# Kernel tuning notes

Measured on AMD Instinct MI355X. Metric: run time of the kernel, lower is better.

Reference implementation:

```python
import jax, jax.numpy as jnp
import numpy as np

# ---- Cl(4,1) Cayley table (conformal GA: metric +,+,+,+,-) ----
_METRIC = (1.0, 1.0, 1.0, 1.0, -1.0)

def _reorder_sign(a, b):
    # sign from counting swaps to bring blade product to canonical order
    a >>= 1
    s = 0
    while a:
        s += bin(a & b).count("1")
        a >>= 1
    return -1.0 if (s & 1) else 1.0

def _build_cayley():
    C = np.zeros((32, 32, 32), dtype=np.float32)
    for a in range(32):
        for b in range(32):
            s = _reorder_sign(a, b)
            common = a & b
            for i in range(5):
                if (common >> i) & 1:
                    s *= _METRIC[i]
            C[a, b, a ^ b] += s
    return C

CAYLEY = _build_cayley()  # [32,32,32]; out_k = sum_ij C[i,j,k] x_i y_j

EPS = 1e-8

def normalize_cl41(x):
    n = jnp.sqrt(jnp.sum(x * x, axis=-1, keepdims=True))
    return x / (n + EPS)


def setup_inputs() -> dict:
    key = jax.random.key(0)
    k_x, k_wi, k_bi, k_wo, k_bo = jax.random.split(key, 5)
    B, S, D, H = 64, 2048, 6, 8
    x = jax.random.normal(k_x, (B, S, D), dtype=jnp.float32)
    W_in = jax.random.normal(k_wi, (D, H * 32), dtype=jnp.float32) * (1.0 / np.sqrt(D))
    b_in = jax.random.normal(k_bi, (H * 32,), dtype=jnp.float32) * 0.01
    W_out = jax.random.normal(k_wo, (H * 32, 32), dtype=jnp.float32) * (1.0 / np.sqrt(H * 32))
    b_out = jax.random.normal(k_bo, (32,), dtype=jnp.float32) * 0.01
    return {"x": x, "W_in": W_in, "b_in": b_in, "W_out": W_out, "b_out": b_out}


def reference(x, W_in, b_in, W_out, b_out):
    B, S, D = x.shape
    H = W_in.shape[1] // 32
    C = jnp.asarray(CAYLEY)
    # project inputs to per-channel multivectors: (B,S,H,32)
    u = (x @ W_in + b_in).reshape(B, S, H, 32)
    # initial rotor state: identity (scalar blade = 1)
    psi0 = jnp.zeros((B, H, 32), dtype=x.dtype).at[..., 0].set(1.0)

    def step(psi, u_t):  # u_t: (B,H,32)
        delta = normalize_cl41(u_t.at[..., 0].add(1.0))
        psi = normalize_cl41(jnp.einsum("bhi,bhj,ijk->bhk", delta, psi, C))
        return psi, psi

    _, psi_seq = jax.lax.scan(step, psi0, jnp.swapaxes(u, 0, 1))  # (S,B,H,32)
    out = normalize_cl41(psi_seq.reshape(S, B, H * 32) @ W_out + b_out)  # (S,B,32)
    return jnp.swapaxes(out, 0, 1)  # (B,S,32)
```

## Files before the change

kernel.cpp:

```cpp
#include <hip/hip_runtime.h>
#include <hip/hip_bf16.h>
#include <stdint.h>

#define BB 64
#define SS 2048
#define DD 6
#define HH 8
#define NCH 512
#define CHUNKS 256
#define LCH 8

typedef unsigned short ushort_t;
typedef __attribute__((ext_vector_type(8))) __bf16 bf16x8;
typedef __attribute__((ext_vector_type(4))) float f32x4;

struct SignTab { float s[32][32]; };

constexpr int popc5_c(unsigned v) {
    int c = 0;
    for (int i = 0; i < 5; ++i) c += (v >> i) & 1u;
    return c;
}

constexpr SignTab make_signs() {
    SignTab t{};
    for (int a = 0; a < 32; ++a) {
        for (int b = 0; b < 32; ++b) {
            int cnt = 0;
            unsigned aa = ((unsigned)a) >> 1;
            while (aa) { cnt += popc5_c(aa & (unsigned)b); aa >>= 1; }
            if ((a & b) & 16) cnt += 1;
            t.s[a][b] = (cnt & 1) ? -1.0f : 1.0f;
        }
    }
    return t;
}

constexpr SignTab SGN = make_signs();

__device__ __forceinline__ void gp_cl41(const float* __restrict__ a,
                                        const float* __restrict__ b,
                                        float* __restrict__ o) {
#pragma unroll
    for (int k = 0; k < 32; ++k) o[k] = 0.0f;
#pragma unroll
    for (int i = 0; i < 32; ++i) {
#pragma unroll
        for (int k = 0; k < 32; ++k) {
            o[k] = fmaf(SGN.s[i][i ^ k] * a[i], b[i ^ k], o[k]);
        }
    }
}

__device__ __forceinline__ float sumsq32(const float* v) {
    float n0 = 0.f, n1 = 0.f, n2 = 0.f, n3 = 0.f;
#pragma unroll
    for (int k = 0; k < 32; k += 4) {
        n0 = fmaf(v[k+0], v[k+0], n0);
        n1 = fmaf(v[k+1], v[k+1], n1);
        n2 = fmaf(v[k+2], v[k+2], n2);
        n3 = fmaf(v[k+3], v[k+3], n3);
    }
    return (n0 + n1) + (n2 + n3);
}

__device__ __forceinline__ float rsq(float n) {
    return __builtin_amdgcn_rsqf(n);
}

__device__ __forceinline__ uint32_t f2bf_rne(float f) {
    uint32_t u = __float_as_uint(f);
    return (u + 0x7FFFu + ((u >> 16) & 1u)) >> 16;
}

__device__ __forceinline__ void make_delta2(const float4* __restrict__ sW,
                                            const float* __restrict__ xv,
                                            float* __restrict__ dl0,
                                            float* __restrict__ dl1) {
#pragma unroll
    for (int j4 = 0; j4 < 8; ++j4) {
        float4 bv = sW[48 + j4];
        dl0[4*j4+0] = bv.x; dl0[4*j4+1] = bv.y; dl0[4*j4+2] = bv.z; dl0[4*j4+3] = bv.w;
        dl1[4*j4+0] = bv.x; dl1[4*j4+1] = bv.y; dl1[4*j4+2] = bv.z; dl1[4*j4+3] = bv.w;
    }
#pragma unroll
    for (int d = 0; d < 6; ++d) {
        float a0 = xv[d], a1 = xv[6 + d];
#pragma unroll
        for (int j4 = 0; j4 < 8; ++j4) {
            float4 w = sW[d * 8 + j4];
            dl0[4*j4+0] = fmaf(a0, w.x, dl0[4*j4+0]);
            dl0[4*j4+1] = fmaf(a0, w.y, dl0[4*j4+1]);
            dl0[4*j4+2] = fmaf(a0, w.z, dl0[4*j4+2]);
            dl0[4*j4+3] = fmaf(a0, w.w, dl0[4*j4+3]);
            dl1[4*j4+0] = fmaf(a1, w.x, dl1[4*j4+0]);
            dl1[4*j4+1] = fmaf(a1, w.y, dl1[4*j4+1]);
            dl1[4*j4+2] = fmaf(a1, w.z, dl1[4*j4+2]);
            dl1[4*j4+3] = fmaf(a1, w.w, dl1[4*j4+3]);
        }
    }
    dl0[0] += 1.0f;
    dl1[0] += 1.0f;
}

__device__ __forceinline__ void loadx12(const float* __restrict__ xr, float* __restrict__ xv) {
    const float4* xp = (const float4*)xr;
#pragma unroll
    for (int m = 0; m < 3; ++m) {
        float4 t4 = xp[m];
        xv[4*m] = t4.x; xv[4*m+1] = t4.y; xv[4*m+2] = t4.z; xv[4*m+3] = t4.w;
    }
}

__global__ __launch_bounds__(256, 1) void k_scan(
        const float* __restrict__ x, const float* __restrict__ W_in,
        const float* __restrict__ b_in, float* __restrict__ Ebuf) {
    __shared__ float4 sW4[57];
    __shared__ float sT[CHUNKS][36];

    int chain = blockIdx.x;
    int b = chain >> 3, h = chain & 7;
    int c = threadIdx.x;

    if (c < 56) {
        float4 v;
        if (c < 48) {
            int d = c / 8, j4 = c % 8;
            const float* p = W_in + d * 256 + h * 32 + 4 * j4;
            v = make_float4(p[0], p[1], p[2], p[3]);
        } else {
            const float* p = b_in + h * 32 + 4 * (c - 48);
            v = make_float4(p[0], p[1], p[2], p[3]);
        }
        sW4[c] = v;
    }
    __syncthreads();

    const float* xrow = x + ((size_t)b * SS + (size_t)c * LCH) * DD;
    float P[32], O[32];
    {
        float xv[12];
        loadx12(xrow, xv);
        float dl0[32], dl1[32];
        make_delta2(sW4, xv, dl0, dl1);
        gp_cl41(dl1, dl0, P);
    }
#pragma unroll 1
    for (int pr = 1; pr < 4; ++pr) {
        float xv[12];
        loadx12(xrow + 12 * pr, xv);
        float dl0[32], dl1[32];
        make_delta2(sW4, xv, dl0, dl1);
        gp_cl41(dl0, P, O);
        gp_cl41(dl1, O, P);
    }

    float v[32];
    {
        float inv = rsq(sumsq32(P));
#pragma unroll
        for (int k = 0; k < 32; ++k) v[k] = P[k] * inv;
#pragma unroll
        for (int m = 0; m < 8; ++m)
            *(float4*)&sT[c][4*m] = make_float4(v[4*m], v[4*m+1], v[4*m+2], v[4*m+3]);
    }
    __syncthreads();

#pragma unroll 1
    for (int off = 1; off < CHUNKS; off <<= 1) {
        float w[32];
        bool act = (c >= off);
        if (act) {
#pragma unroll
            for (int m = 0; m < 8; ++m) {
                float4 t4 = *(const float4*)&sT[c - off][4*m];
                w[4*m] = t4.x; w[4*m+1] = t4.y; w[4*m+2] = t4.z; w[4*m+3] = t4.w;
            }
        }
        __syncthreads();
        if (act) {
            gp_cl41(v, w, O);
            float inv = rsq(sumsq32(O));
#pragma unroll
            for (int k = 0; k < 32; ++k) v[k] = O[k] * inv;
#pragma unroll
            for (int m = 0; m < 8; ++m)
                *(float4*)&sT[c][4*m] = make_float4(v[4*m], v[4*m+1], v[4*m+2], v[4*m+3]);
        }
        __syncthreads();
    }

    float* dst = Ebuf + (size_t)chain * CHUNKS * 32;
    if (c == 0) {
        *(float4*)dst = make_float4(1.f, 0.f, 0.f, 0.f);
#pragma unroll
        for (int m = 1; m < 8; ++m) *(float4*)(dst + 4*m) = make_float4(0.f, 0.f, 0.f, 0.f);
    }
    if (c < CHUNKS - 1) {
        float* d2 = dst + (size_t)(c + 1) * 32;
#pragma unroll
        for (int m = 0; m < 8; ++m)
            *(float4*)(d2 + 4*m) = make_float4(v[4*m], v[4*m+1], v[4*m+2], v[4*m+3]);
    }
}

__global__ __launch_bounds__(256, 1) void k_chain_proj(
        const float* __restrict__ x, const float* __restrict__ W_in,
        const float* __restrict__ b_in, const float* __restrict__ Ebuf,
        const float* __restrict__ W_out, const float* __restrict__ b_out,
        float* __restrict__ out) {
    __shared__ float4 sW4[8][57];
    __shared__ float sX[1536];
    __shared__ ushort_t Wt[32 * 256];
    __shared__ ushort_t psiT[4 * 16 * 256];

    int tid = threadIdx.x;
    int wv = tid >> 6, lane = tid & 63;
    int b = blockIdx.x >> 3, gq = blockIdx.x & 7;
    int grp = gq * 4 + wv;
    int c0 = grp * 8;
    int cl = lane >> 3, h = lane & 7;
    int q = lane >> 4, n0 = lane & 15;

    float4 pv[8];
    {
        const float4* ep = (const float4*)(Ebuf +
                (((size_t)b * HH + h) * CHUNKS + (c0 + cl)) * 32);
#pragma unroll
        for (int m = 0; m < 8; ++m) pv[m] = ep[m];
    }

    for (int idx = tid; idx < 448; idx += 256) {
        int hh = idx / 56, r = idx % 56;
        float4 v;
        if (r < 48) {
            int d = r / 8, j4 = r % 8;
            const float* p = W_in + d * 256 + hh * 32 + 4 * j4;
            v = make_float4(p[0], p[1], p[2], p[3]);
        } else {
            const float* p = b_in + hh * 32 + 4 * (r - 48);
            v = make_float4(p[0], p[1], p[2], p[3]);
        }
        sW4[hh][r] = v;
    }

    {
        const float4* xp = (const float4*)(x + ((size_t)b * SS + (size_t)gq * 256) * DD);
        float4* sx4 = (float4*)sX;
        for (int idx = tid; idx < 384; idx += 256) sx4[idx] = xp[idx];
    }

    for (int idx = tid; idx < 2048; idx += 256) {
        int k = idx >> 3, n4 = (idx & 7) << 2;
        float4 w4 = ((const float4*)W_out)[idx];
        ushort_t vals[4] = { (ushort_t)f2bf_rne(w4.x), (ushort_t)f2bf_rne(w4.y),
                             (ushort_t)f2bf_rne(w4.z), (ushort_t)f2bf_rne(w4.w) };
#pragma unroll
        for (int j = 0; j < 4; ++j) {
            int n = n4 + j;
            uint32_t off = (uint32_t)(n * 512 + 2 * k) ^ (uint32_t)((n & 7) << 4);
            *(ushort_t*)((char*)Wt + off) = vals[j];
        }
    }
    __syncthreads();

    float p[32];
#pragma unroll
    for (int m = 0; m < 8; ++m) {
        p[4*m] = pv[m].x; p[4*m+1] = pv[m].y; p[4*m+2] = pv[m].z; p[4*m+3] = pv[m].w;
    }

    bf16x8 Bf[2][8];
#pragma unroll
    for (int nt = 0; nt < 2; ++nt) {
        int n = nt * 16 + n0;
        uint32_t rb = (uint32_t)(n * 512);
        uint32_t sw = (uint32_t)((n & 7) << 4);
#pragma unroll
        for (int kk = 0; kk < 8; ++kk)
            Bf[nt][kk] = *(const bf16x8*)((const char*)Wt + ((rb + kk * 64 + q * 16) ^ sw));
    }
    float bn0 = b_out[n0], bn1 = b_out[16 + n0];

    ushort_t* myT = psiT + wv * 16 * 256;

#pragma unroll 1
    for (int pr = 0; pr < 4; ++pr) {
        float xv[12];
        {
            const float* xr = sX + (wv * 64 + cl * 8 + 2 * pr) * 6;
#pragma unroll
            for (int d = 0; d < 12; ++d) xv[d] = xr[d];
        }

        float dl0[32], dl1[32], o[32];
        make_delta2(sW4[h], xv, dl0, dl1);

        gp_cl41(dl0, p, o);
        {
            float inv = rsq(sumsq32(o));
            int row = cl * 2;
            uint32_t rb = (uint32_t)(row * 512 + h * 64);
            uint32_t sw = (uint32_t)((row & 7) << 4);
            uint32_t pk[16];
#pragma unroll
            for (int m = 0; m < 16; ++m)
                pk[m] = f2bf_rne(o[2*m] * inv) | (f2bf_rne(o[2*m+1] * inv) << 16);
#pragma unroll
            for (int m = 0; m < 4; ++m)
                *(uint4*)((char*)myT + ((rb + 16 * m) ^ sw)) =
                    make_uint4(pk[4*m], pk[4*m+1], pk[4*m+2], pk[4*m+3]);
        }
        gp_cl41(dl1, o, p);
        {
            float inv = rsq(sumsq32(p));
            int row = cl * 2 + 1;
            uint32_t rb = (uint32_t)(row * 512 + h * 64);
            uint32_t sw = (uint32_t)((row & 7) << 4);
            uint32_t pk[16];
#pragma unroll
            for (int m = 0; m < 16; ++m)
                pk[m] = f2bf_rne(p[2*m] * inv) | (f2bf_rne(p[2*m+1] * inv) << 16);
#pragma unroll
            for (int m = 0; m < 4; ++m)
                *(uint4*)((char*)myT + ((rb + 16 * m) ^ sw)) =
                    make_uint4(pk[4*m], pk[4*m+1], pk[4*m+2], pk[4*m+3]);
        }

        __syncthreads();

        f32x4 acc0 = {0.f, 0.f, 0.f, 0.f};
        f32x4 acc1 = {0.f, 0.f, 0.f, 0.f};
        {
            uint32_t rb = (uint32_t)(n0 * 512);
            uint32_t sw = (uint32_t)((n0 & 7) << 4);
#pragma unroll
            for (int kk = 0; kk < 8; ++kk) {
                bf16x8 af = *(const bf16x8*)((const char*)myT + ((rb + kk * 64 + q * 16) ^ sw));
                acc0 = __builtin_amdgcn_mfma_f32_16x16x32_bf16(af, Bf[0][kk], acc0, 0, 0, 0);
                acc1 = __builtin_amdgcn_mfma_f32_16x16x32_bf16(af, Bf[1][kk], acc1, 0, 0, 0);
            }
        }

        float c0v[4], c1v[4], ssq[4];
#pragma unroll
        for (int i = 0; i < 4; ++i) {
            c0v[i] = acc0[i] + bn0;
            c1v[i] = acc1[i] + bn1;
            ssq[i] = c0v[i] * c0v[i] + c1v[i] * c1v[i];
        }
#pragma unroll
        for (int m = 1; m < 16; m <<= 1) {
#pragma unroll
            for (int i = 0; i < 4; ++i) ssq[i] += __shfl_xor(ssq[i], m);
        }
#pragma unroll
        for (int i = 0; i < 4; ++i) {
            float inv = rsq(ssq[i]);
            int mrow = q * 4 + i;
            int s = (c0 + (mrow >> 1)) * LCH + 2 * pr + (mrow & 1);
            size_t row = (size_t)b * SS + s;
            out[row * 32 + n0]      = c0v[i] * inv;
            out[row * 32 + 16 + n0] = c1v[i] * inv;
        }

        __syncthreads();
    }
}

extern "C" void kernel_launch(void* const* d_in, const int* in_sizes, int n_in,
                              void* d_out, int out_size, void* d_ws, size_t ws_size,
                              hipStream_t stream) {
    const float* x     = (const float*)d_in[0];
    const float* W_in  = (const float*)d_in[1];
    const float* b_in  = (const float*)d_in[2];
    const float* W_out = (const float*)d_in[3];
    const float* b_out = (const float*)d_in[4];
    float* out = (float*)d_out;

    float* Ebuf = (float*)d_ws;

    k_scan      <<<NCH, 256, 0, stream>>>(x, W_in, b_in, Ebuf);
    k_chain_proj<<<NCH, 256, 0, stream>>>(x, W_in, b_in, Ebuf, W_out, b_out, out);
}
```

Baseline: 174.5 us.

## Trim scan normalizations, drop last barrier step, use wave-local LDS fences

```diff
diff --git a/kernel.cpp b/kernel.cpp
--- a/kernel.cpp
+++ b/kernel.cpp
@@ -13,6 +13,10 @@
 typedef unsigned short ushort_t;
 typedef __attribute__((ext_vector_type(8))) __bf16 bf16x8;
 typedef __attribute__((ext_vector_type(4))) float f32x4;
+
+#define WAVE_LDS_FENCE() do { \
+    asm volatile("s_waitcnt lgkmcnt(0)" ::: "memory"); \
+    __builtin_amdgcn_sched_barrier(0); } while (0)
 
 struct SignTab { float s[32][32]; };
 
@@ -166,8 +170,9 @@
     }
     __syncthreads();
 
+    int rr = 0;
 #pragma unroll 1
-    for (int off = 1; off < CHUNKS; off <<= 1) {
+    for (int off = 1; off < 128; off <<= 1, ++rr) {
         float w[32];
         bool act = (c >= off);
         if (act) {
@@ -180,14 +185,31 @@
         __syncthreads();
         if (act) {
             gp_cl41(v, w, O);
-            float inv = rsq(sumsq32(O));
-#pragma unroll
-            for (int k = 0; k < 32; ++k) v[k] = O[k] * inv;
+            if (rr & 1) {
+                float inv = rsq(sumsq32(O));
+#pragma unroll
+                for (int k = 0; k < 32; ++k) v[k] = O[k] * inv;
+            } else {
+#pragma unroll
+                for (int k = 0; k < 32; ++k) v[k] = O[k];
+            }
 #pragma unroll
             for (int m = 0; m < 8; ++m)
                 *(float4*)&sT[c][4*m] = make_float4(v[4*m], v[4*m+1], v[4*m+2], v[4*m+3]);
         }
         __syncthreads();
+    }
+
+    if (c >= 128) {
+        float w[32];
+#pragma unroll
+        for (int m = 0; m < 8; ++m) {
+            float4 t4 = *(const float4*)&sT[c - 128][4*m];
+            w[4*m] = t4.x; w[4*m+1] = t4.y; w[4*m+2] = t4.z; w[4*m+3] = t4.w;
+        }
+        gp_cl41(v, w, O);
+#pragma unroll
+        for (int k = 0; k < 32; ++k) v[k] = O[k];
     }
 
     float* dst = Ebuf + (size_t)chain * CHUNKS * 32;
@@ -197,10 +219,12 @@
         for (int m = 1; m < 8; ++m) *(float4*)(dst + 4*m) = make_float4(0.f, 0.f, 0.f, 0.f);
     }
     if (c < CHUNKS - 1) {
+        float inv = rsq(sumsq32(v));
         float* d2 = dst + (size_t)(c + 1) * 32;
 #pragma unroll
         for (int m = 0; m < 8; ++m)
-            *(float4*)(d2 + 4*m) = make_float4(v[4*m], v[4*m+1], v[4*m+2], v[4*m+3]);
+            *(float4*)(d2 + 4*m) = make_float4(v[4*m] * inv, v[4*m+1] * inv,
+                                               v[4*m+2] * inv, v[4*m+3] * inv);
     }
 }
 
@@ -289,8 +313,7 @@
         float xv[12];
         {
             const float* xr = sX + (wv * 64 + cl * 8 + 2 * pr) * 6;
-#pragma unroll
-            for (int d = 0; d < 12; ++d) xv[d] = xr[d];
+            loadx12(xr, xv);
         }
 
         float dl0[32], dl1[32], o[32];
@@ -327,7 +350,7 @@
                     make_uint4(pk[4*m], pk[4*m+1], pk[4*m+2], pk[4*m+3]);
         }
 
-        __syncthreads();
+        WAVE_LDS_FENCE();
 
         f32x4 acc0 = {0.f, 0.f, 0.f, 0.f};
         f32x4 acc1 = {0.f, 0.f, 0.f, 0.f};
@@ -364,7 +387,7 @@
             out[row * 32 + 16 + n0] = c1v[i] * inv;
         }
 
-        __syncthreads();
+        WAVE_LDS_FENCE();
     }
 }
 
```

Result: no change. 173.8 us (-0.4%).
